# Kernel tuning notes

Measured on AMD Instinct MI355X. Metric: run time of the kernel, lower is better.

Reference implementation:

```python
import jax, jax.numpy as jnp
import numpy as np

B, N, EMBED, CHEB_K, INP, HID = 32, 8192, 16, 2, 2, 64


def setup_inputs() -> dict:
    key = jax.random.key(0)
    k1, k2, k3, k4 = jax.random.split(key, 4)
    return {
        "x": jax.random.normal(k1, (B, N, INP), dtype=jnp.float32),
        "adj": jax.random.normal(k2, (N, EMBED), dtype=jnp.float32),
        "weights_pool": jax.random.normal(k3, (EMBED, CHEB_K, INP, HID), dtype=jnp.float32) * 0.1,
        "bias_pool": jax.random.normal(k4, (EMBED, HID), dtype=jnp.float32) * 0.1,
    }


def reference(x, adj, weights_pool, bias_pool):
    n = adj.shape[0]
    cheb_k = weights_pool.shape[1]
    # adaptive adjacency: row-softmax of relu(E E^T)
    ADJ = jax.nn.softmax(jax.nn.relu(adj @ adj.T), axis=1)  # [n, n]
    support_set = [jnp.eye(n, dtype=x.dtype), ADJ]
    for k in range(2, cheb_k):  # Chebyshev recursion (fixed small k)
        support_set.append(2.0 * ADJ @ support_set[-1] - support_set[-2])
    supports = jnp.stack(support_set, axis=0)  # [k, n, n]
    # node-adaptive weights / bias
    weights = jnp.einsum("nd,dkio->nkio", adj, weights_pool)  # [n,k,inp,hid]
    bias = adj @ bias_pool  # [n, hid]
    # graph propagation, directly in bnkc layout (fuses the permute)
    x_g = jnp.einsum("knm,bmc->bnkc", supports, x)  # [b,n,k,inp]
    out = jnp.einsum("bnki,nkio->bno", x_g, weights) + bias  # [b,n,hid]
    return out
```

## Files before the change

kernel.cpp:

```cpp
#include <hip/hip_runtime.h>

#define NN 8192
#define BB 32
#define EMB 16
#define HID 64
#define VCOLS 64
#define MS 16
#define TN 128
#define TM 64
#define VT_PITCH 8192

typedef __attribute__((ext_vector_type(8))) short bf16x8;
typedef __attribute__((ext_vector_type(4))) float f32x4;

static __device__ inline short f2b(float f) {
    union { float f; unsigned u; } v; v.f = f;
    unsigned r = (v.u + 0x7fffu + ((v.u >> 16) & 1u)) >> 16;
    return (short)r;
}

__global__ void k_build(const float* __restrict__ x, const float* __restrict__ adj,
                        short* __restrict__ VT, short* __restrict__ adjB) {
    int t = threadIdx.x;
    if (blockIdx.x < 512) {
        int idx = blockIdx.x * 256 + t;
        int b = idx >> 12;
        int m = (idx & 4095) * 2;
        float4 xx = *(const float4*)(x + (size_t)b * NN * 2 + 2 * m);
        unsigned u0 = (unsigned short)f2b(xx.x) | ((unsigned)(unsigned short)f2b(xx.z) << 16);
        unsigned u1 = (unsigned short)f2b(xx.y) | ((unsigned)(unsigned short)f2b(xx.w) << 16);
        *(unsigned*)(VT + (size_t)(2 * b) * VT_PITCH + m) = u0;
        *(unsigned*)(VT + (size_t)(2 * b + 1) * VT_PITCH + m) = u1;
    } else {
        int idx = (blockIdx.x - 512) * 256 + t;
        float4 aa = *(const float4*)(adj + (size_t)idx * 4);
        unsigned u0 = (unsigned short)f2b(aa.x) | ((unsigned)(unsigned short)f2b(aa.y) << 16);
        unsigned u1 = (unsigned short)f2b(aa.z) | ((unsigned)(unsigned short)f2b(aa.w) << 16);
        uint2 uu; uu.x = u0; uu.y = u1;
        *(uint2*)(adjB + (size_t)idx * 4) = uu;
    }
}

__launch_bounds__(256, 4)
__global__ void k_prop(const short* __restrict__ adjB, const short* __restrict__ VT,
                       float* __restrict__ ynum, float* __restrict__ den) {
    __shared__ char smraw[128 * 68 * 4];
    short* adjT = (short*)smraw;
    short* vt   = (short*)(smraw + 2048);
    float* OL   = (float*)smraw;

    const int t = threadIdx.x;
    const int wv = t >> 6;
    const int lane = t & 63;
    const int l = lane & 15;
    const int q = lane >> 4;
    const int n0 = blockIdx.x * TN;
    const int mbeg = blockIdx.y * (NN / MS);

    bf16x8 Bn[2];
    bf16x8 zv = {0, 0, 0, 0, 0, 0, 0, 0};
#pragma unroll
    for (int s = 0; s < 2; ++s) {
        const short* src = adjB + (size_t)(n0 + 32 * wv + 16 * s + l) * EMB + (q & 1) * 8;
        bf16x8 v = *(const bf16x8*)src;
        Bn[s] = (q < 2) ? v : zv;
    }

    f32x4 acc[4][2];
#pragma unroll
    for (int u = 0; u < 4; ++u)
#pragma unroll
        for (int s = 0; s < 2; ++s) {
            acc[u][s][0] = 0.f; acc[u][s][1] = 0.f; acc[u][s][2] = 0.f; acc[u][s][3] = 0.f;
        }
    float dsum[2] = {0.f, 0.f};
    const int mrow_b = 8 * (l >> 2) + (l & 3);

    for (int m0 = mbeg; m0 < mbeg + (NN / MS); m0 += TM) {
        __syncthreads();
        if (t < 128) {
            int row = t >> 1, g = t & 1;
            *(bf16x8*)(adjT + row * 16 + ((g ^ (row & 1)) * 8)) =
                *(const bf16x8*)(adjB + (size_t)m0 * EMB + t * 8);
        }
#pragma unroll
        for (int cc = 0; cc < 2; ++cc) {
            int id = t * 2 + cc;
            int j = id >> 3;
            int g = id & 7;
            int gs = (g + (j & 7)) & 7;
            *(bf16x8*)(vt + j * 72 + gs * 8) =
                *(const bf16x8*)(VT + (size_t)j * VT_PITCH + m0 + g * 8);
        }
        __syncthreads();

#pragma unroll
        for (int c = 0; c < 2; ++c) {
            short pe0[8], pe1[8];
#pragma unroll
            for (int h = 0; h < 2; ++h) {
                int mrow = mrow_b + 32 * c + 4 * h;
                bf16x8 Af = *(const bf16x8*)(adjT + mrow * 16 + (((q & 1) ^ (mrow & 1)) * 8));
                f32x4 z = {0.f, 0.f, 0.f, 0.f};
                f32x4 S0 = __builtin_amdgcn_mfma_f32_16x16x32_bf16(Af, Bn[0], z, 0, 0, 0);
                f32x4 S1 = __builtin_amdgcn_mfma_f32_16x16x32_bf16(Af, Bn[1], z, 0, 0, 0);
#pragma unroll
                for (int r = 0; r < 4; ++r) {
                    float p0 = __expf(fmaxf(S0[r], 0.f));
                    float p1 = __expf(fmaxf(S1[r], 0.f));
                    dsum[0] += p0; dsum[1] += p1;
                    pe0[4 * h + r] = f2b(p0);
                    pe1[4 * h + r] = f2b(p1);
                }
            }
            bf16x8 pf0 = {pe0[0], pe0[1], pe0[2], pe0[3], pe0[4], pe0[5], pe0[6], pe0[7]};
            bf16x8 pf1 = {pe1[0], pe1[1], pe1[2], pe1[3], pe1[4], pe1[5], pe1[6], pe1[7]};
#pragma unroll
            for (int u = 0; u < 4; ++u) {
                int row = 16 * u + l;
                int gs = ((4 * c + q) + (l & 7)) & 7;
                bf16x8 Vf = *(const bf16x8*)(vt + row * 72 + gs * 8);
                acc[u][0] = __builtin_amdgcn_mfma_f32_16x16x32_bf16(Vf, pf0, acc[u][0], 0, 0, 0);
                acc[u][1] = __builtin_amdgcn_mfma_f32_16x16x32_bf16(Vf, pf1, acc[u][1], 0, 0, 0);
            }
        }
    }

#pragma unroll
    for (int s = 0; s < 2; ++s) {
        float d = dsum[s];
        d += __shfl_xor(d, 16);
        d += __shfl_xor(d, 32);
        if (q == 0) atomicAdd(den + (n0 + 32 * wv + 16 * s + l), d);
    }

    __syncthreads();
#pragma unroll
    for (int u = 0; u < 4; ++u)
#pragma unroll
        for (int s = 0; s < 2; ++s)
#pragma unroll
            for (int r = 0; r < 4; ++r)
                OL[(32 * wv + 16 * s + l) * 68 + 16 * u + 4 * q + r] = acc[u][s][r];
    __syncthreads();
    for (int rr = 0; rr < 32; ++rr) {
        int nloc = 32 * wv + rr;
        atomicAdd(ynum + (size_t)(n0 + nloc) * 64 + lane, OL[nloc * 68 + lane]);
    }
}

__global__ void k_epi(const float* __restrict__ adj, const float* __restrict__ wp,
                      const float* __restrict__ bp, const float* __restrict__ x,
                      const float* __restrict__ ynum, const float* __restrict__ den,
                      float* __restrict__ out) {
    const int n = blockIdx.x;
    const int o = threadIdx.x;
    __shared__ float xl[VCOLS];
    __shared__ float yl[VCOLS];

    float an[EMB];
#pragma unroll
    for (int d = 0; d < EMB; ++d) an[d] = adj[n * EMB + d];

    float W00 = 0.f, W01 = 0.f, W10 = 0.f, W11 = 0.f, bias = 0.f;
#pragma unroll
    for (int d = 0; d < EMB; ++d) {
        float a = an[d];
        W00 += a * wp[((d * 2 + 0) * 2 + 0) * HID + o];
        W01 += a * wp[((d * 2 + 0) * 2 + 1) * HID + o];
        W10 += a * wp[((d * 2 + 1) * 2 + 0) * HID + o];
        W11 += a * wp[((d * 2 + 1) * 2 + 1) * HID + o];
        bias += a * bp[d * HID + o];
    }

    float rden = 1.f / den[n];
    yl[o] = ynum[(size_t)n * VCOLS + o] * rden;
    xl[o] = x[(o >> 1) * (NN * 2) + n * 2 + (o & 1)];
    __syncthreads();

#pragma unroll 4
    for (int b = 0; b < BB; ++b) {
        float v = xl[2 * b] * W00 + xl[2 * b + 1] * W01
                + yl[2 * b] * W10 + yl[2 * b + 1] * W11 + bias;
        out[((size_t)b * NN + n) * HID + o] = v;
    }
}

extern "C" void kernel_launch(void* const* d_in, const int* in_sizes, int n_in,
                              void* d_out, int out_size, void* d_ws, size_t ws_size,
                              hipStream_t stream) {
    const float* x   = (const float*)d_in[0];
    const float* adj = (const float*)d_in[1];
    const float* wp  = (const float*)d_in[2];
    const float* bp  = (const float*)d_in[3];
    float* out = (float*)d_out;

    char* w = (char*)d_ws;
    short* VT   = (short*)w;
    short* adjB = (short*)(w + (size_t)64 * VT_PITCH * 2);
    float* ynum = (float*)(w + (size_t)64 * VT_PITCH * 2 + (size_t)NN * EMB * 2);
    float* den  = ynum + (size_t)NN * VCOLS;

    hipMemsetAsync(ynum, 0, ((size_t)NN * VCOLS + NN) * sizeof(float), stream);
    k_build<<<640, 256, 0, stream>>>(x, adj, VT, adjB);
    k_prop<<<dim3(NN / TN, MS), 256, 0, stream>>>(adjB, VT, ynum, den);
    k_epi<<<NN, 64, 0, stream>>>(adj, wp, bp, x, ynum, den, out);
}
```

Before: 130.2 us.

## Restructure propagation: direct global fragment loads, MFMA row sums, split-K partial buffers

The propagation kernel now loads adjacency and value fragments straight from global memory into registers, with no LDS staging or barriers. Each wave covers 64 nodes instead of 32. The softmax denominator is computed with an MFMA against a ones vector, exp uses exp2 on adjacency pre-scaled by log2(e), and the bf16 pack becomes simple truncation. Atomics and the memset are replaced by per-split partial buffers that the epilogue reduces, and the node-adaptive weights are precomputed in a separate kernel. This removes LDS traffic, synchronisation and atomic contention, at the cost of more register pressure, a bigger workspace, and the epilogue reading 16 partial slices.

```diff
diff --git a/kernel.cpp b/kernel.cpp
--- a/kernel.cpp
+++ b/kernel.cpp
@@ -4,9 +4,8 @@
 #define BB 32
 #define EMB 16
 #define HID 64
-#define VCOLS 64
 #define MS 16
-#define TN 128
+#define TNB 256
 #define TM 64
 #define VT_PITCH 8192
 
@@ -20,7 +19,8 @@
 }
 
 __global__ void k_build(const float* __restrict__ x, const float* __restrict__ adj,
-                        short* __restrict__ VT, short* __restrict__ adjB) {
+                        short* __restrict__ VT, short* __restrict__ adjB,
+                        short* __restrict__ adjS) {
     int t = threadIdx.x;
     if (blockIdx.x < 512) {
         int idx = blockIdx.x * 256 + t;
@@ -32,157 +32,176 @@
         *(unsigned*)(VT + (size_t)(2 * b) * VT_PITCH + m) = u0;
         *(unsigned*)(VT + (size_t)(2 * b + 1) * VT_PITCH + m) = u1;
     } else {
+        const float L2E = 1.4426950408889634f;
         int idx = (blockIdx.x - 512) * 256 + t;
         float4 aa = *(const float4*)(adj + (size_t)idx * 4);
-        unsigned u0 = (unsigned short)f2b(aa.x) | ((unsigned)(unsigned short)f2b(aa.y) << 16);
-        unsigned u1 = (unsigned short)f2b(aa.z) | ((unsigned)(unsigned short)f2b(aa.w) << 16);
-        uint2 uu; uu.x = u0; uu.y = u1;
-        *(uint2*)(adjB + (size_t)idx * 4) = uu;
-    }
-}
-
-__launch_bounds__(256, 4)
-__global__ void k_prop(const short* __restrict__ adjB, const short* __restrict__ VT,
+        uint2 ub, us;
+        ub.x = (unsigned short)f2b(aa.x) | ((unsigned)(unsigned short)f2b(aa.y) << 16);
+        ub.y = (unsigned short)f2b(aa.z) | ((unsigned)(unsigned short)f2b(aa.w) << 16);
+        us.x = (unsigned short)f2b(aa.x * L2E) | ((unsigned)(unsigned short)f2b(aa.y * L2E) << 16);
+        us.y = (unsigned short)f2b(aa.z * L2E) | ((unsigned)(unsigned short)f2b(aa.w * L2E) << 16);
+        *(uint2*)(adjB + (size_t)idx * 4) = ub;
+        *(uint2*)(adjS + (size_t)idx * 4) = us;
+    }
+}
+
+__global__ void k_weights(const float* __restrict__ adj, const float* __restrict__ wp,
+                          const float* __restrict__ bp, float* __restrict__ Wbuf) {
+    const int nl = threadIdx.x >> 4, og = threadIdx.x & 15;
+    const int n = blockIdx.x * 16 + nl;
+    const float4* wp4 = (const float4*)wp;
+    const float4* bp4 = (const float4*)bp;
+    float an[EMB];
+#pragma unroll
+    for (int d = 0; d < EMB; ++d) an[d] = adj[n * EMB + d];
+    float4 w[5];
+#pragma unroll
+    for (int c = 0; c < 5; ++c) { w[c].x = w[c].y = w[c].z = w[c].w = 0.f; }
+#pragma unroll
+    for (int d = 0; d < EMB; ++d) {
+        float a = an[d];
+#pragma unroll
+        for (int c = 0; c < 4; ++c) {
+            float4 p = wp4[(d * 4 + c) * 16 + og];
+            w[c].x += a * p.x; w[c].y += a * p.y; w[c].z += a * p.z; w[c].w += a * p.w;
+        }
+        float4 pb = bp4[d * 16 + og];
+        w[4].x += a * pb.x; w[4].y += a * pb.y; w[4].z += a * pb.z; w[4].w += a * pb.w;
+    }
+#pragma unroll
+    for (int c = 0; c < 5; ++c)
+        *(float4*)(Wbuf + (size_t)n * 320 + c * 64 + og * 4) = w[c];
+}
+
+__launch_bounds__(256, 2)
+__global__ void k_prop(const short* __restrict__ adjB, const short* __restrict__ adjS,
+                       const short* __restrict__ VT,
                        float* __restrict__ ynum, float* __restrict__ den) {
-    __shared__ char smraw[128 * 68 * 4];
-    short* adjT = (short*)smraw;
-    short* vt   = (short*)(smraw + 2048);
-    float* OL   = (float*)smraw;
-
     const int t = threadIdx.x;
     const int wv = t >> 6;
     const int lane = t & 63;
     const int l = lane & 15;
     const int q = lane >> 4;
-    const int n0 = blockIdx.x * TN;
+    const int n0 = blockIdx.x * TNB + wv * 64;
     const int mbeg = blockIdx.y * (NN / MS);
 
-    bf16x8 Bn[2];
+    bf16x8 Bn[4];
     bf16x8 zv = {0, 0, 0, 0, 0, 0, 0, 0};
 #pragma unroll
-    for (int s = 0; s < 2; ++s) {
-        const short* src = adjB + (size_t)(n0 + 32 * wv + 16 * s + l) * EMB + (q & 1) * 8;
+    for (int s = 0; s < 4; ++s) {
+        const short* src = adjS + (size_t)(n0 + 16 * s + l) * EMB + (q & 1) * 8;
         bf16x8 v = *(const bf16x8*)src;
         Bn[s] = (q < 2) ? v : zv;
     }
-
-    f32x4 acc[4][2];
+    const short one = (short)0x3F80;
+    bf16x8 ones = {one, one, one, one, one, one, one, one};
+
+    f32x4 acc[4][4];
+    f32x4 dacc[4];
 #pragma unroll
     for (int u = 0; u < 4; ++u)
 #pragma unroll
-        for (int s = 0; s < 2; ++s) {
-            acc[u][s][0] = 0.f; acc[u][s][1] = 0.f; acc[u][s][2] = 0.f; acc[u][s][3] = 0.f;
-        }
-    float dsum[2] = {0.f, 0.f};
+        for (int s = 0; s < 4; ++s) { acc[u][s][0] = acc[u][s][1] = acc[u][s][2] = acc[u][s][3] = 0.f; }
+#pragma unroll
+    for (int s = 0; s < 4; ++s) { dacc[s][0] = dacc[s][1] = dacc[s][2] = dacc[s][3] = 0.f; }
+
     const int mrow_b = 8 * (l >> 2) + (l & 3);
 
     for (int m0 = mbeg; m0 < mbeg + (NN / MS); m0 += TM) {
-        __syncthreads();
-        if (t < 128) {
-            int row = t >> 1, g = t & 1;
-            *(bf16x8*)(adjT + row * 16 + ((g ^ (row & 1)) * 8)) =
-                *(const bf16x8*)(adjB + (size_t)m0 * EMB + t * 8);
-        }
-#pragma unroll
-        for (int cc = 0; cc < 2; ++cc) {
-            int id = t * 2 + cc;
-            int j = id >> 3;
-            int g = id & 7;
-            int gs = (g + (j & 7)) & 7;
-            *(bf16x8*)(vt + j * 72 + gs * 8) =
-                *(const bf16x8*)(VT + (size_t)j * VT_PITCH + m0 + g * 8);
-        }
-        __syncthreads();
+        bf16x8 Af[2][2], Vf[2][4];
+#pragma unroll
+        for (int c = 0; c < 2; ++c)
+#pragma unroll
+            for (int h = 0; h < 2; ++h)
+                Af[c][h] = *(const bf16x8*)(adjB + (size_t)(m0 + 32 * c + mrow_b + 4 * h) * EMB + (q & 1) * 8);
+#pragma unroll
+        for (int c = 0; c < 2; ++c)
+#pragma unroll
+            for (int u = 0; u < 4; ++u)
+                Vf[c][u] = *(const bf16x8*)(VT + (size_t)(16 * u + l) * VT_PITCH + m0 + 32 * c + q * 8);
 
 #pragma unroll
         for (int c = 0; c < 2; ++c) {
-            short pe0[8], pe1[8];
-#pragma unroll
-            for (int h = 0; h < 2; ++h) {
-                int mrow = mrow_b + 32 * c + 4 * h;
-                bf16x8 Af = *(const bf16x8*)(adjT + mrow * 16 + (((q & 1) ^ (mrow & 1)) * 8));
-                f32x4 z = {0.f, 0.f, 0.f, 0.f};
-                f32x4 S0 = __builtin_amdgcn_mfma_f32_16x16x32_bf16(Af, Bn[0], z, 0, 0, 0);
-                f32x4 S1 = __builtin_amdgcn_mfma_f32_16x16x32_bf16(Af, Bn[1], z, 0, 0, 0);
+            f32x4 z = {0.f, 0.f, 0.f, 0.f};
+            f32x4 S0[4], S1[4];
+#pragma unroll
+            for (int s = 0; s < 4; ++s) {
+                S0[s] = __builtin_amdgcn_mfma_f32_16x16x32_bf16(Af[c][0], Bn[s], z, 0, 0, 0);
+                S1[s] = __builtin_amdgcn_mfma_f32_16x16x32_bf16(Af[c][1], Bn[s], z, 0, 0, 0);
+            }
+#pragma unroll
+            for (int s = 0; s < 4; ++s) {
+                unsigned wb[8];
 #pragma unroll
                 for (int r = 0; r < 4; ++r) {
-                    float p0 = __expf(fmaxf(S0[r], 0.f));
-                    float p1 = __expf(fmaxf(S1[r], 0.f));
-                    dsum[0] += p0; dsum[1] += p1;
-                    pe0[4 * h + r] = f2b(p0);
-                    pe1[4 * h + r] = f2b(p1);
+                    union { float f; unsigned u; } p0, p1;
+                    p0.f = __builtin_amdgcn_exp2f(fmaxf(S0[s][r], 0.f));
+                    p1.f = __builtin_amdgcn_exp2f(fmaxf(S1[s][r], 0.f));
+                    wb[r] = p0.u;
+                    wb[4 + r] = p1.u;
                 }
-            }
-            bf16x8 pf0 = {pe0[0], pe0[1], pe0[2], pe0[3], pe0[4], pe0[5], pe0[6], pe0[7]};
-            bf16x8 pf1 = {pe1[0], pe1[1], pe1[2], pe1[3], pe1[4], pe1[5], pe1[6], pe1[7]};
-#pragma unroll
-            for (int u = 0; u < 4; ++u) {
-                int row = 16 * u + l;
-                int gs = ((4 * c + q) + (l & 7)) & 7;
-                bf16x8 Vf = *(const bf16x8*)(vt + row * 72 + gs * 8);
-                acc[u][0] = __builtin_amdgcn_mfma_f32_16x16x32_bf16(Vf, pf0, acc[u][0], 0, 0, 0);
-                acc[u][1] = __builtin_amdgcn_mfma_f32_16x16x32_bf16(Vf, pf1, acc[u][1], 0, 0, 0);
+                union { bf16x8 v; unsigned d[4]; } pf;
+#pragma unroll
+                for (int dd = 0; dd < 4; ++dd)
+                    pf.d[dd] = (wb[2 * dd + 1] & 0xFFFF0000u) | (wb[2 * dd] >> 16);
+#pragma unroll
+                for (int u = 0; u < 4; ++u)
+                    acc[u][s] = __builtin_amdgcn_mfma_f32_16x16x32_bf16(Vf[c][u], pf.v, acc[u][s], 0, 0, 0);
+                dacc[s] = __builtin_amdgcn_mfma_f32_16x16x32_bf16(ones, pf.v, dacc[s], 0, 0, 0);
             }
         }
     }
 
-#pragma unroll
-    for (int s = 0; s < 2; ++s) {
-        float d = dsum[s];
-        d += __shfl_xor(d, 16);
-        d += __shfl_xor(d, 32);
-        if (q == 0) atomicAdd(den + (n0 + 32 * wv + 16 * s + l), d);
-    }
-
-    __syncthreads();
-#pragma unroll
-    for (int u = 0; u < 4; ++u)
-#pragma unroll
-        for (int s = 0; s < 2; ++s)
-#pragma unroll
-            for (int r = 0; r < 4; ++r)
-                OL[(32 * wv + 16 * s + l) * 68 + 16 * u + 4 * q + r] = acc[u][s][r];
-    __syncthreads();
-    for (int rr = 0; rr < 32; ++rr) {
-        int nloc = 32 * wv + rr;
-        atomicAdd(ynum + (size_t)(n0 + nloc) * 64 + lane, OL[nloc * 68 + lane]);
-    }
-}
-
-__global__ void k_epi(const float* __restrict__ adj, const float* __restrict__ wp,
-                      const float* __restrict__ bp, const float* __restrict__ x,
+    float* yp = ynum + (size_t)blockIdx.y * NN * HID;
+#pragma unroll
+    for (int s = 0; s < 4; ++s) {
+#pragma unroll
+        for (int u = 0; u < 4; ++u)
+            *(f32x4*)(yp + (size_t)(n0 + 16 * s + l) * HID + 16 * u + 4 * q) = acc[u][s];
+        if (q == 0) den[(size_t)blockIdx.y * NN + n0 + 16 * s + l] = dacc[s][0];
+    }
+}
+
+__global__ void k_epi(const float* __restrict__ Wbuf, const float* __restrict__ x,
                       const float* __restrict__ ynum, const float* __restrict__ den,
                       float* __restrict__ out) {
-    const int n = blockIdx.x;
-    const int o = threadIdx.x;
-    __shared__ float xl[VCOLS];
-    __shared__ float yl[VCOLS];
-
-    float an[EMB];
-#pragma unroll
-    for (int d = 0; d < EMB; ++d) an[d] = adj[n * EMB + d];
-
-    float W00 = 0.f, W01 = 0.f, W10 = 0.f, W11 = 0.f, bias = 0.f;
-#pragma unroll
-    for (int d = 0; d < EMB; ++d) {
-        float a = an[d];
-        W00 += a * wp[((d * 2 + 0) * 2 + 0) * HID + o];
-        W01 += a * wp[((d * 2 + 0) * 2 + 1) * HID + o];
-        W10 += a * wp[((d * 2 + 1) * 2 + 0) * HID + o];
-        W11 += a * wp[((d * 2 + 1) * 2 + 1) * HID + o];
-        bias += a * bp[d * HID + o];
-    }
-
-    float rden = 1.f / den[n];
-    yl[o] = ynum[(size_t)n * VCOLS + o] * rden;
-    xl[o] = x[(o >> 1) * (NN * 2) + n * 2 + (o & 1)];
+    const int nl = threadIdx.x >> 4, og = threadIdx.x & 15;
+    const int n = blockIdx.x * 16 + nl;
+    __shared__ float xl[16][68];
+    __shared__ float yl[16][68];
+
+    float4 W[5];
+#pragma unroll
+    for (int c = 0; c < 5; ++c)
+        W[c] = *(const float4*)(Wbuf + (size_t)n * 320 + c * 64 + og * 4);
+
+    float4 ysum; ysum.x = ysum.y = ysum.z = ysum.w = 0.f;
+    float dsum = 0.f;
+#pragma unroll
+    for (int s = 0; s < MS; ++s) {
+        float4 p = *(const float4*)(ynum + ((size_t)s * NN + n) * HID + og * 4);
+        ysum.x += p.x; ysum.y += p.y; ysum.z += p.z; ysum.w += p.w;
+        dsum += den[(size_t)s * NN + n];
+    }
+    float rden = 1.f / dsum;
+    *(float4*)&yl[nl][og * 4] = make_float4(ysum.x * rden, ysum.y * rden, ysum.z * rden, ysum.w * rden);
+
+    float2 x0 = *(const float2*)(x + ((size_t)(og * 2) * NN + n) * 2);
+    float2 x1 = *(const float2*)(x + ((size_t)(og * 2 + 1) * NN + n) * 2);
+    xl[nl][og * 4 + 0] = x0.x; xl[nl][og * 4 + 1] = x0.y;
+    xl[nl][og * 4 + 2] = x1.x; xl[nl][og * 4 + 3] = x1.y;
     __syncthreads();
 
 #pragma unroll 4
     for (int b = 0; b < BB; ++b) {
-        float v = xl[2 * b] * W00 + xl[2 * b + 1] * W01
-                + yl[2 * b] * W10 + yl[2 * b + 1] * W11 + bias;
-        out[((size_t)b * NN + n) * HID + o] = v;
+        float xb0 = xl[nl][2 * b], xb1 = xl[nl][2 * b + 1];
+        float yb0 = yl[nl][2 * b], yb1 = yl[nl][2 * b + 1];
+        float4 o4;
+        o4.x = xb0 * W[0].x + xb1 * W[1].x + yb0 * W[2].x + yb1 * W[3].x + W[4].x;
+        o4.y = xb0 * W[0].y + xb1 * W[1].y + yb0 * W[2].y + yb1 * W[3].y + W[4].y;
+        o4.z = xb0 * W[0].z + xb1 * W[1].z + yb0 * W[2].z + yb1 * W[3].z + W[4].z;
+        o4.w = xb0 * W[0].w + xb1 * W[1].w + yb0 * W[2].w + yb1 * W[3].w + W[4].w;
+        *(float4*)(out + ((size_t)b * NN + n) * HID + og * 4) = o4;
     }
 }
 
@@ -197,12 +216,14 @@
 
     char* w = (char*)d_ws;
     short* VT   = (short*)w;
-    short* adjB = (short*)(w + (size_t)64 * VT_PITCH * 2);
-    float* ynum = (float*)(w + (size_t)64 * VT_PITCH * 2 + (size_t)NN * EMB * 2);
-    float* den  = ynum + (size_t)NN * VCOLS;
-
-    hipMemsetAsync(ynum, 0, ((size_t)NN * VCOLS + NN) * sizeof(float), stream);
-    k_build<<<640, 256, 0, stream>>>(x, adj, VT, adjB);
-    k_prop<<<dim3(NN / TN, MS), 256, 0, stream>>>(adjB, VT, ynum, den);
-    k_epi<<<NN, 64, 0, stream>>>(adj, wp, bp, x, ynum, den, out);
-}
+    short* adjB = (short*)(w + (size_t)2 * 64 * VT_PITCH);
+    short* adjS = adjB + (size_t)NN * EMB;
+    float* Wbuf = (float*)(w + (size_t)2 * 64 * VT_PITCH + (size_t)4 * NN * EMB);
+    float* ynum = Wbuf + (size_t)NN * 320;
+    float* den  = ynum + (size_t)MS * NN * HID;
+
+    k_build<<<640, 256, 0, stream>>>(x, adj, VT, adjB, adjS);
+    k_weights<<<NN / 16, 256, 0, stream>>>(adj, wp, bp, Wbuf);
+    k_prop<<<dim3(NN / TNB, MS), 256, 0, stream>>>(adjB, adjS, VT, ynum, den);
+    k_epi<<<NN / 16, 256, 0, stream>>>(Wbuf, x, ynum, den, out);
+}
```

Result: slower. 141.5 us (+8.7%).
